# Kernel tuning notes

Hardware: AMD Instinct MI355X
Metric: run time of the kernel (lower is better)

Reference implementation:

```python
import jax, jax.numpy as jnp
import numpy as np

L = 3000          # nodes per modality
M = 3             # modalities
N = L * M         # total nodes
E = 200000        # edges
D = 512           # hidden_dim
S = D // 4        # shared_dim = 128
EPS = 1e-12       # F.normalize eps


def _lrelu(x):
    return jax.nn.leaky_relu(x, negative_slope=0.01)


def _l2norm(x):
    n = jnp.linalg.norm(x, axis=-1, keepdims=True)
    return x / jnp.maximum(n, EPS)


def setup_inputs() -> dict:
    key = jax.random.key(0)
    ks = jax.random.split(key, 16)
    w = lambda k, shape: (jax.random.normal(k, shape, dtype=jnp.float32) * 0.02)
    inp = {
        "feat0": jax.random.normal(ks[0], (L, D), dtype=jnp.float32),
        "feat1": jax.random.normal(ks[1], (L, D), dtype=jnp.float32),
        "feat2": jax.random.normal(ks[2], (L, D), dtype=jnp.float32),
        "edge_index": jax.random.randint(ks[3], (2, E), 0, N, dtype=jnp.int64),
        # EdgeWeightGen params (torch Linear convention: weight is (out, in))
        "proj_w": w(ks[4], (S, D)),
        "mlp_w1": w(ks[5], (S, 2 * S)),
        "mlp_b1": jnp.zeros((S,), dtype=jnp.float32),
        "mlp_w2": w(ks[6], (1, S)),
        "mlp_b2": jnp.zeros((1,), dtype=jnp.float32),
        # CrossModalGraphLayer params, 2 layers
        "W1_0": w(ks[7], (D, D)),
        "W2_0": w(ks[8], (D, 2 * D)),
        "W1_1": w(ks[9], (D, D)),
        "W2_1": w(ks[10], (D, 2 * D)),
    }
    return inp


def reference(feat0, feat1, feat2, edge_index, proj_w, mlp_w1, mlp_b1,
              mlp_w2, mlp_b2, W1_0, W2_0, W1_1, W2_1):
    feature = jnp.concatenate([feat0, feat1, feat2], axis=0)  # (N, D)
    src, tgt = edge_index[0], edge_index[1]

    # EdgeWeightGen
    shared_src = _l2norm(feature[src] @ proj_w.T)   # (E, S)
    shared_tgt = _l2norm(feature[tgt] @ proj_w.T)   # (E, S)
    emb_cat = jnp.concatenate([shared_src, shared_tgt], axis=-1)  # (E, 2S)
    h = _lrelu(emb_cat @ mlp_w1.T + mlp_b1)
    edge_weight = jax.nn.sigmoid((h @ mlp_w2.T + mlp_b2)[:, 0])   # (E,)

    # build_adj_matrix: dense scatter-add (sparse_coo coalesce sums dups)
    adj = jnp.zeros((N, N), dtype=feature.dtype).at[src, tgt].add(edge_weight)
    row_sum = adj.sum(axis=1)
    d_inv_sqrt = jnp.where(row_sum > 0, row_sum ** -0.5, 0.0)
    # D^{-1/2} A D^{-1/2} as elementwise row/col scaling (same math as diag matmuls)
    gcn = d_inv_sqrt[:, None] * adj * d_inv_sqrt[None, :]

    # graph layers
    x = feature
    for W1, W2 in ((W1_0, W2_0), (W1_1, W2_1)):
        proj = x @ W1.T                 # (N, D)
        nb = gcn @ proj                 # (N, D)
        cat = jnp.concatenate([x + nb, x * nb], axis=-1)  # (N, 2D)
        x = _lrelu(cat @ W2.T)
    return x  # concatenated updated features; chunk(x, 3) recovers per-modal tuple
```

## Files before the change

kernel.cpp:

```cpp
#include <hip/hip_runtime.h>
#include <hip/hip_bf16.h>
#include <math.h>

#define NL 3000
#define NN 9000
#define NE 200000
#define DD 512
#define SS 128
#define MPAD 9088
#define MT   (MPAD/16)

typedef __attribute__((ext_vector_type(8))) short    bf16x8;
typedef __attribute__((ext_vector_type(8))) ushort   u16x8;
typedef __attribute__((ext_vector_type(4))) float    f32x4;

static __device__ __forceinline__ ushort f2bf(float f){
  unsigned u = __float_as_uint(f);
  return (ushort)((u + 0x7FFFu + ((u>>16)&1u)) >> 16);
}
static __device__ __forceinline__ float bf2f(ushort u){
  return __uint_as_float(((unsigned)u)<<16);
}

__global__ __launch_bounds__(256) void k_packall(const float* __restrict__ f0, const float* __restrict__ f1,
                        const float* __restrict__ f2, const float* __restrict__ pw,
                        const float* __restrict__ w1,
                        const float* __restrict__ W10, const float* __restrict__ W20,
                        const float* __restrict__ W11, const float* __restrict__ W21,
                        const int* __restrict__ src,
                        short* __restrict__ Ap1, short* __restrict__ BpF,
                        short* __restrict__ Bp10, short* __restrict__ Bp20,
                        short* __restrict__ Bp11, short* __restrict__ Bp21,
                        short* __restrict__ Bpab,
                        float* __restrict__ row_sum, int* __restrict__ cnt){
  int b = blockIdx.x;
  int lane = threadIdx.x & 63;
  if (b < 2272){
    int t = b*4 + (threadIdx.x>>6);
    int tm = t >> 4, tk = t & 15;
    int m = tm*16 + (lane&15);
    int k = tk*32 + (lane>>4)*8;
    float4 v0 = make_float4(0,0,0,0), v1 = v0;
    if (m < NN){
      const float* srow = (m < NL) ? f0 + (size_t)m*DD
                         : (m < 2*NL) ? f1 + (size_t)(m-NL)*DD
                         : f2 + (size_t)(m-2*NL)*DD;
      v0 = *(const float4*)(srow + k);
      v1 = *(const float4*)(srow + k + 4);
    }
    u16x8 r;
    r[0]=f2bf(v0.x); r[1]=f2bf(v0.y); r[2]=f2bf(v0.z); r[3]=f2bf(v0.w);
    r[4]=f2bf(v1.x); r[5]=f2bf(v1.y); r[6]=f2bf(v1.z); r[7]=f2bf(v1.w);
    *(u16x8*)(Ap1 + (size_t)t*512 + lane*8) = r;
  } else if (b < 3072){
    int t = (b-2272)*4 + (threadIdx.x>>6);
    const float* X; short* P; int K, ntk, lt;
    if (t < 128)      { X=pw;  P=BpF;  K=512;  ntk=16; lt=t; }
    else if (t < 640) { X=W10; P=Bp10; K=512;  ntk=16; lt=t-128; }
    else if (t < 1664){ X=W20; P=Bp20; K=1024; ntk=32; lt=t-640; }
    else if (t < 2176){ X=W11; P=Bp11; K=512;  ntk=16; lt=t-1664; }
    else              { X=W21; P=Bp21; K=1024; ntk=32; lt=t-2176; }
    int tm = lt/ntk, tk = lt - tm*ntk;
    int m = tm*16 + (lane&15);
    int k = tk*32 + (lane>>4)*8;
    float4 v0 = *(const float4*)(X + (size_t)m*K + k);
    float4 v1 = *(const float4*)(X + (size_t)m*K + k + 4);
    u16x8 r;
    r[0]=f2bf(v0.x); r[1]=f2bf(v0.y); r[2]=f2bf(v0.z); r[3]=f2bf(v0.w);
    r[4]=f2bf(v1.x); r[5]=f2bf(v1.y); r[6]=f2bf(v1.z); r[7]=f2bf(v1.w);
    *(u16x8*)(P + (size_t)lt*512 + lane*8) = r;
  } else if (b < 3088){
    int t = (b-3072)*4 + (threadIdx.x>>6);
    int tn = t >> 2, tk = t & 3;
    int n = tn*16 + (lane&15);
    int k = tk*32 + (lane>>4)*8;
    const float* sp = (n<128) ? (w1 + (size_t)n*256 + k) : (w1 + (size_t)(n-128)*256 + 128 + k);
    float4 v0 = *(const float4*)sp;
    float4 v1 = *(const float4*)(sp+4);
    u16x8 r;
    r[0]=f2bf(v0.x); r[1]=f2bf(v0.y); r[2]=f2bf(v0.z); r[3]=f2bf(v0.w);
    r[4]=f2bf(v1.x); r[5]=f2bf(v1.y); r[6]=f2bf(v1.z); r[7]=f2bf(v1.w);
    *(u16x8*)(Bpab + (size_t)t*512 + lane*8) = r;
  } else {
    int idx = (b-3088)*256 + threadIdx.x;
    for (int i=idx; i<NN; i+=8192) row_sum[i]=0.f;
    for (int e=idx; e<NE; e+=8192) atomicAdd(&cnt[src[e]],1);
  }
}

__global__ __launch_bounds__(256) void k_pack(const float* __restrict__ X, short* __restrict__ P,
                                              int M, int K, int nTilesK){
  int t = blockIdx.x*4 + (threadIdx.x>>6);
  int lane = threadIdx.x & 63;
  int tm = t / nTilesK, tk = t - tm*nTilesK;
  int m = tm*16 + (lane&15);
  int k = tk*32 + (lane>>4)*8;
  float4 v0 = make_float4(0,0,0,0), v1 = v0;
  if (m < M){
    v0 = *(const float4*)(X + (size_t)m*K + k);
    v1 = *(const float4*)(X + (size_t)m*K + k + 4);
  }
  u16x8 r;
  r[0]=f2bf(v0.x); r[1]=f2bf(v0.y); r[2]=f2bf(v0.z); r[3]=f2bf(v0.w);
  r[4]=f2bf(v1.x); r[5]=f2bf(v1.y); r[6]=f2bf(v1.z); r[7]=f2bf(v1.w);
  *(u16x8*)(P + (size_t)t*512 + lane*8) = r;
}

template<int ACT, int OBF>
__global__ __launch_bounds__(256) void k_gmm(const short* __restrict__ Ap, const short* __restrict__ Bp,
                                             void* __restrict__ Cv, int M, int N, int K){
  int l = blockIdx.x;
  int rr = l & 7, tt = l >> 3;
  int q = tt % 9, x = tt / 9;
  int y = q*8 + rr;
  if (y >= 71) return;
  int lane = threadIdx.x & 63, wave = threadIdx.x >> 6;
  int ktiles = K >> 5;
  int bm = y*128 + wave*32;
  int bn = x*64;
  const bf16x8* a0 = (const bf16x8*)(Ap + ((size_t)((bm>>4)  ) * ktiles)*512 + lane*8);
  const bf16x8* a1 = (const bf16x8*)(Ap + ((size_t)((bm>>4)+1) * ktiles)*512 + lane*8);
  const bf16x8* b0 = (const bf16x8*)(Bp + ((size_t)((bn>>4)  ) * ktiles)*512 + lane*8);
  const bf16x8* b1 = (const bf16x8*)(Bp + ((size_t)((bn>>4)+1) * ktiles)*512 + lane*8);
  const bf16x8* b2 = (const bf16x8*)(Bp + ((size_t)((bn>>4)+2) * ktiles)*512 + lane*8);
  const bf16x8* b3 = (const bf16x8*)(Bp + ((size_t)((bn>>4)+3) * ktiles)*512 + lane*8);
  f32x4 acc[2][4];
  #pragma unroll
  for (int i=0;i<2;++i)
    #pragma unroll
    for (int j=0;j<4;++j) acc[i][j] = (f32x4){0.f,0.f,0.f,0.f};

  for (int kt=0; kt<ktiles; ++kt){
    int off = kt*64;
    bf16x8 A0 = a0[off], A1 = a1[off];
    bf16x8 B0 = b0[off], B1 = b1[off], B2 = b2[off], B3 = b3[off];
    acc[0][0] = __builtin_amdgcn_mfma_f32_16x16x32_bf16(A0, B0, acc[0][0], 0,0,0);
    acc[0][1] = __builtin_amdgcn_mfma_f32_16x16x32_bf16(A0, B1, acc[0][1], 0,0,0);
    acc[0][2] = __builtin_amdgcn_mfma_f32_16x16x32_bf16(A0, B2, acc[0][2], 0,0,0);
    acc[0][3] = __builtin_amdgcn_mfma_f32_16x16x32_bf16(A0, B3, acc[0][3], 0,0,0);
    acc[1][0] = __builtin_amdgcn_mfma_f32_16x16x32_bf16(A1, B0, acc[1][0], 0,0,0);
    acc[1][1] = __builtin_amdgcn_mfma_f32_16x16x32_bf16(A1, B1, acc[1][1], 0,0,0);
    acc[1][2] = __builtin_amdgcn_mfma_f32_16x16x32_bf16(A1, B2, acc[1][2], 0,0,0);
    acc[1][3] = __builtin_amdgcn_mfma_f32_16x16x32_bf16(A1, B3, acc[1][3], 0,0,0);
  }
  int colo = lane & 15;
  int rowo = (lane >> 4) * 4;
  #pragma unroll
  for (int mi=0; mi<2; ++mi){
    #pragma unroll
    for (int r=0; r<4; ++r){
      int row = bm + mi*16 + rowo + r;
      if (row < M){
        #pragma unroll
        for (int ni=0; ni<4; ++ni){
          float v = acc[mi][ni][r];
          if (ACT) v = v>0.f ? v : 0.01f*v;
          int cidx = bn + ni*16 + colo;
          if (OBF) ((ushort*)Cv)[(size_t)row*N + cidx] = f2bf(v);
          else     ((float*) Cv)[(size_t)row*N + cidx] = v;
        }
      }
    }
  }
}

__global__ __launch_bounds__(256) void k_l2n(const float* __restrict__ X, short* __restrict__ ShP){
  int lane = threadIdx.x & 63, wave = threadIdx.x >> 6;
  int m = blockIdx.x*4 + wave;
  float2 v = ((const float2*)(X + (size_t)m*SS))[lane];
  float ss = v.x*v.x + v.y*v.y;
  #pragma unroll
  for (int o=32;o>0;o>>=1) ss += __shfl_xor(ss, o);
  float inv = 1.f / fmaxf(sqrtf(ss), 1e-12f);
  int k = 2*lane;
  int tIdx = (m>>4)*4 + (k>>5);
  int pos  = ((m&15) + ((k>>3)&3)*16)*8 + (k&7);
  ushort2 r; r.x = f2bf(v.x*inv); r.y = f2bf(v.y*inv);
  *(ushort2*)(ShP + (size_t)tIdx*512 + pos) = r;
}

__global__ __launch_bounds__(256) void k_edge(const int* __restrict__ src, const int* __restrict__ tgt,
                      const ushort* __restrict__ AB,
                      const float* __restrict__ b1, const float* __restrict__ w2,
                      const float* __restrict__ b2p,
                      const int* __restrict__ row_ptr, int* __restrict__ fill,
                      int* __restrict__ col, float* __restrict__ ewC,
                      float* __restrict__ row_sum){
  int lane = threadIdx.x & 63;
  int p = lane & 15, g = lane >> 4;
  int wid = blockIdx.x*(blockDim.x>>6) + (threadIdx.x>>6);
  int nw  = gridDim.x*(blockDim.x>>6);
  float4 b1a = ((const float4*)b1)[p*2], b1b = ((const float4*)b1)[p*2+1];
  float4 w2a = ((const float4*)w2)[p*2], w2b = ((const float4*)w2)[p*2+1];
  float bb[8] = {b1a.x,b1a.y,b1a.z,b1a.w,b1b.x,b1b.y,b1b.z,b1b.w};
  float ww[8] = {w2a.x,w2a.y,w2a.z,w2a.w,w2b.x,w2b.y,w2b.z,w2b.w};
  float b2 = b2p[0];
  for (int e = wid*4+g; e < NE; e += nw*4){
    int s = src[e], tg_ = tgt[e];
    u16x8 av = *(const u16x8*)(AB + (size_t)s*256 + p*8);
    u16x8 bv = *(const u16x8*)(AB + (size_t)tg_*256 + 128 + p*8);
    float acc = 0.f;
    #pragma unroll
    for (int i=0;i<8;++i){
      float h = bf2f(av[i]) + bf2f(bv[i]) + bb[i];
      h = h>0.f ? h : 0.01f*h;
      acc += h*ww[i];
    }
    acc += __shfl_xor(acc,1); acc += __shfl_xor(acc,2);
    acc += __shfl_xor(acc,4); acc += __shfl_xor(acc,8);
    if (p==0){
      float wgt = 1.f/(1.f+expf(-(acc+b2)));
      int pos = atomicAdd(&fill[s],1);
      int idx = row_ptr[s]+pos;
      col[idx]=tg_;
      ewC[idx]=wgt;
      atomicAdd(&row_sum[s], wgt);
    }
  }
}

__global__ __launch_bounds__(1024) void k_scan(const int* __restrict__ cnt,
                      int* __restrict__ row_ptr, int* __restrict__ fill){
  __shared__ int wsum[16];
  int t = threadIdx.x;
  int lane = t & 63, wid = t >> 6;
  const int CH = 9;
  int base = t*CH;
  int v[CH]; int s = 0;
  #pragma unroll
  for (int i=0;i<CH;++i){
    int idx = base+i;
    v[i] = (idx<NN) ? cnt[idx] : 0;
    s += v[i];
  }
  int ps = s;
  #pragma unroll
  for (int o=1;o<64;o<<=1){
    int x = __shfl_up(ps, o);
    if (lane >= o) ps += x;
  }
  if (lane==63) wsum[wid] = ps;
  __syncthreads();
  if (wid==0){
    int wv = (lane<16)? wsum[lane] : 0;
    #pragma unroll
    for (int o=1;o<16;o<<=1){
      int x = __shfl_up(wv, o);
      if (lane>=o) wv += x;
    }
    if (lane<16) wsum[lane]=wv;
  }
  __syncthreads();
  int prefix = (wid>0 ? wsum[wid-1] : 0) + (ps - s);
  #pragma unroll
  for (int i=0;i<CH;++i){
    int idx = base+i;
    if (idx<NN){
      row_ptr[idx] = prefix;
      fill[idx] = 0;
      prefix += v[i];
    }
  }
  if (t==1023) row_ptr[NN] = wsum[15];
}

template<int LAYER>
__global__ __launch_bounds__(128) void k_spmm_cat(const int* __restrict__ row_ptr, const int* __restrict__ col,
                     const float* __restrict__ ew, const float* __restrict__ row_sum,
                     const ushort* __restrict__ proj,
                     const float* __restrict__ xf0, const float* __restrict__ xf1,
                     const float* __restrict__ xf2,
                     short* __restrict__ P){
  int m = blockIdx.x, t = threadIdx.x;
  int beg = row_ptr[m], end = row_ptr[m+1];
  float rsm = row_sum[m];
  float dim = rsm>0.f ? rsqrtf(rsm) : 0.f;
  float4 a0 = make_float4(0,0,0,0), a1 = a0, a2 = a0, a3 = a0;
  int j = beg;
  for (; j+4<=end; j+=4){
    int c0=col[j], c1=col[j+1], c2=col[j+2], c3=col[j+3];
    float r0=row_sum[c0], r1=row_sum[c1], r2=row_sum[c2], r3=row_sum[c3];
    float w0=ew[j]  *(r0>0.f?rsqrtf(r0):0.f);
    float w1=ew[j+1]*(r1>0.f?rsqrtf(r1):0.f);
    float w2_=ew[j+2]*(r2>0.f?rsqrtf(r2):0.f);
    float w3=ew[j+3]*(r3>0.f?rsqrtf(r3):0.f);
    ushort4 p0 = ((const ushort4*)(proj + (size_t)c0*DD))[t];
    ushort4 p1 = ((const ushort4*)(proj + (size_t)c1*DD))[t];
    ushort4 p2 = ((const ushort4*)(proj + (size_t)c2*DD))[t];
    ushort4 p3 = ((const ushort4*)(proj + (size_t)c3*DD))[t];
    a0.x += w0*bf2f(p0.x); a0.y += w0*bf2f(p0.y); a0.z += w0*bf2f(p0.z); a0.w += w0*bf2f(p0.w);
    a1.x += w1*bf2f(p1.x); a1.y += w1*bf2f(p1.y); a1.z += w1*bf2f(p1.z); a1.w += w1*bf2f(p1.w);
    a2.x += w2_*bf2f(p2.x); a2.y += w2_*bf2f(p2.y); a2.z += w2_*bf2f(p2.z); a2.w += w2_*bf2f(p2.w);
    a3.x += w3*bf2f(p3.x); a3.y += w3*bf2f(p3.y); a3.z += w3*bf2f(p3.z); a3.w += w3*bf2f(p3.w);
  }
  for (; j<end; ++j){
    int c0=col[j];
    float r0=row_sum[c0];
    float w0=ew[j]*(r0>0.f?rsqrtf(r0):0.f);
    ushort4 p0 = ((const ushort4*)(proj + (size_t)c0*DD))[t];
    a0.x += w0*bf2f(p0.x); a0.y += w0*bf2f(p0.y); a0.z += w0*bf2f(p0.z); a0.w += w0*bf2f(p0.w);
  }
  a0.x = dim*(a0.x + a1.x + a2.x + a3.x);
  a0.y = dim*(a0.y + a1.y + a2.y + a3.y);
  a0.z = dim*(a0.z + a1.z + a2.z + a3.z);
  a0.w = dim*(a0.w + a1.w + a2.w + a3.w);
  const float* xrow;
  if (LAYER==0){
    xrow = (m < NL) ? xf0 + (size_t)m*DD
         : (m < 2*NL) ? xf1 + (size_t)(m-NL)*DD
         : xf2 + (size_t)(m-2*NL)*DD;
  } else {
    xrow = xf0 + (size_t)m*DD;
  }
  float4 xv = ((const float4*)xrow)[t];
  float ax = xv.x + a0.x, ay = xv.y + a0.y, az = xv.z + a0.z, aw = xv.w + a0.w;
  float mx = xv.x * a0.x, my = xv.y * a0.y, mz = xv.z * a0.z, mw = xv.w * a0.w;
  ushort4 ra, rm;
  ra.x=f2bf(ax); ra.y=f2bf(ay); ra.z=f2bf(az); ra.w=f2bf(aw);
  rm.x=f2bf(mx); rm.y=f2bf(my); rm.z=f2bf(mz); rm.w=f2bf(mw);
  size_t tileA = (size_t)((m>>4)*32 + (t>>3));
  int    off   = ((m&15) + ((t>>1)&3)*16)*8 + (t&1)*4;
  *(ushort4*)(P + tileA*512 + off)        = ra;
  *(ushort4*)(P + (tileA+16)*512 + off)   = rm;
}

extern "C" void kernel_launch(void* const* d_in, const int* in_sizes, int n_in,
                              void* d_out, int out_size, void* d_ws, size_t ws_size,
                              hipStream_t stream){
  const float* f0 = (const float*)d_in[0];
  const float* f1 = (const float*)d_in[1];
  const float* f2 = (const float*)d_in[2];
  const int*   ei = (const int*)d_in[3];
  const float* pw = (const float*)d_in[4];
  const float* w1 = (const float*)d_in[5];
  const float* b1 = (const float*)d_in[6];
  const float* w2 = (const float*)d_in[7];
  const float* b2 = (const float*)d_in[8];
  const float* W1_0 = (const float*)d_in[9];
  const float* W2_0 = (const float*)d_in[10];
  const float* W1_1 = (const float*)d_in[11];
  const float* W2_1 = (const float*)d_in[12];
  float* out = (float*)d_out;

  const int* src = ei;
  const int* tgt = ei + NE;

  char* base = (char*)d_ws;
  size_t o = 0;
  auto alloc = [&](size_t bytes)->char*{ char* p = base + o; o += (bytes + 1023) & ~size_t(1023); return p; };
  float* x1      = (float*)alloc((size_t)NN*DD*4);
  ushort* projbf = (ushort*)alloc((size_t)NN*DD*2);
  float* projS   = (float*)alloc((size_t)NN*SS*4);
  ushort* ABn    = (ushort*)alloc((size_t)NN*256*2);
  short* Apack1  = (short*)alloc((size_t)MT*16*1024);
  short* Apack2  = (short*)alloc((size_t)MT*32*1024);
  short* ShP     = (short*)alloc((size_t)MT*4*1024);
  short* BpF     = (short*)alloc((size_t)8*16*1024);
  short* Bpab    = (short*)alloc((size_t)16*4*1024);
  short* Bp10    = (short*)alloc((size_t)32*16*1024);
  short* Bp20    = (short*)alloc((size_t)32*32*1024);
  short* Bp11    = (short*)alloc((size_t)32*16*1024);
  short* Bp21    = (short*)alloc((size_t)32*32*1024);
  float* ew      = (float*)alloc(NE*4);
  float* row_sum = (float*)alloc(NN*4);
  int*   cnt     = (int*)alloc(NN*4);
  int*   fill    = (int*)alloc(NN*4);
  int*   row_ptr = (int*)alloc((NN+1)*4);
  int*   col     = (int*)alloc(NE*4);

  hipMemsetAsync(cnt, 0, NN*4, stream);

  k_packall<<<3120, 256, 0, stream>>>(f0,f1,f2,pw,w1,W1_0,W2_0,W1_1,W2_1,src,
                                      Apack1,BpF,Bp10,Bp20,Bp11,Bp21,Bpab,row_sum,cnt);
  k_scan<<<1, 1024, 0, stream>>>(cnt,row_ptr,fill);

  k_gmm<0,0><<<2*72, 256, 0, stream>>>(Apack1, BpF, projS, NN, 128, 512);
  k_l2n<<<NN/4, 256, 0, stream>>>(projS, ShP);
  k_gmm<0,1><<<4*72, 256, 0, stream>>>(ShP, Bpab, ABn, NN, 256, 128);

  k_edge<<<2048, 256, 0, stream>>>(src,tgt,ABn,b1,w2,b2,row_ptr,fill,col,ew,row_sum);

  k_gmm<0,1><<<8*72, 256, 0, stream>>>(Apack1, Bp10, projbf, NN, DD, DD);
  k_spmm_cat<0><<<NN, 128, 0, stream>>>(row_ptr, col, ew, row_sum, projbf, f0, f1, f2, Apack2);
  k_gmm<1,0><<<8*72, 256, 0, stream>>>(Apack2, Bp20, x1, NN, DD, 2*DD);
  k_pack<<<MT*16/4, 256, 0, stream>>>(x1, Apack1, NN, DD, 16);
  k_gmm<0,1><<<8*72, 256, 0, stream>>>(Apack1, Bp11, projbf, NN, DD, DD);
  k_spmm_cat<1><<<NN, 128, 0, stream>>>(row_ptr, col, ew, row_sum, projbf, x1, nullptr, nullptr, Apack2);
  k_gmm<1,0><<<8*72, 256, 0, stream>>>(Apack2, Bp21, out, NN, DD, 2*DD);
}
```

Baseline: 319.3 us.

## Fuse edge-projection GEMM, L2 norm and MLP GEMM; emit packed bf16 layer output

```diff
diff --git a/kernel.cpp b/kernel.cpp
--- a/kernel.cpp
+++ b/kernel.cpp
@@ -88,22 +88,85 @@
   }
 }
 
-__global__ __launch_bounds__(256) void k_pack(const float* __restrict__ X, short* __restrict__ P,
-                                              int M, int K, int nTilesK){
-  int t = blockIdx.x*4 + (threadIdx.x>>6);
-  int lane = threadIdx.x & 63;
-  int tm = t / nTilesK, tk = t - tm*nTilesK;
-  int m = tm*16 + (lane&15);
-  int k = tk*32 + (lane>>4)*8;
-  float4 v0 = make_float4(0,0,0,0), v1 = v0;
-  if (m < M){
-    v0 = *(const float4*)(X + (size_t)m*K + k);
-    v1 = *(const float4*)(X + (size_t)m*K + k + 4);
-  }
-  u16x8 r;
-  r[0]=f2bf(v0.x); r[1]=f2bf(v0.y); r[2]=f2bf(v0.z); r[3]=f2bf(v0.w);
-  r[4]=f2bf(v1.x); r[5]=f2bf(v1.y); r[6]=f2bf(v1.z); r[7]=f2bf(v1.w);
-  *(u16x8*)(P + (size_t)t*512 + lane*8) = r;
+__global__ __launch_bounds__(256) void k_front(const short* __restrict__ Ap, const short* __restrict__ BpF,
+                                               const short* __restrict__ Bpab, ushort* __restrict__ ABn){
+  __shared__ ushort sh[4][32][136];
+  int lane = threadIdx.x & 63, wave = threadIdx.x >> 6;
+  int bm = blockIdx.x*128 + wave*32;
+  const bf16x8* a0 = (const bf16x8*)(Ap + ((size_t)((bm>>4)  )*16)*512 + lane*8);
+  const bf16x8* a1 = (const bf16x8*)(Ap + ((size_t)((bm>>4)+1)*16)*512 + lane*8);
+  const bf16x8* bp[8];
+  #pragma unroll
+  for (int i=0;i<8;++i) bp[i] = (const bf16x8*)(BpF + ((size_t)i*16)*512 + lane*8);
+  f32x4 acc[2][8];
+  #pragma unroll
+  for (int i=0;i<2;++i)
+    #pragma unroll
+    for (int j=0;j<8;++j) acc[i][j] = (f32x4){0.f,0.f,0.f,0.f};
+  for (int kt=0; kt<16; ++kt){
+    int off = kt*64;
+    bf16x8 A0 = a0[off], A1 = a1[off];
+    #pragma unroll
+    for (int i=0;i<8;++i){
+      bf16x8 Bf = bp[i][off];
+      acc[0][i] = __builtin_amdgcn_mfma_f32_16x16x32_bf16(A0, Bf, acc[0][i], 0,0,0);
+      acc[1][i] = __builtin_amdgcn_mfma_f32_16x16x32_bf16(A1, Bf, acc[1][i], 0,0,0);
+    }
+  }
+  int rowo = (lane>>4)*4, colo = lane & 15;
+  float inv[2][4];
+  #pragma unroll
+  for (int mi=0; mi<2; ++mi){
+    #pragma unroll
+    for (int r=0; r<4; ++r){
+      float s = 0.f;
+      #pragma unroll
+      for (int ni=0; ni<8; ++ni){ float v = acc[mi][ni][r]; s += v*v; }
+      s += __shfl_xor(s,1); s += __shfl_xor(s,2); s += __shfl_xor(s,4); s += __shfl_xor(s,8);
+      inv[mi][r] = 1.f / fmaxf(sqrtf(s), 1e-12f);
+    }
+  }
+  #pragma unroll
+  for (int mi=0; mi<2; ++mi)
+    #pragma unroll
+    for (int r=0; r<4; ++r)
+      #pragma unroll
+      for (int ni=0; ni<8; ++ni)
+        sh[wave][mi*16 + rowo + r][colo + 16*ni] = f2bf(acc[mi][ni][r]*inv[mi][r]);
+  __syncthreads();
+  bf16x8 af[2][4];
+  #pragma unroll
+  for (int mi=0; mi<2; ++mi)
+    #pragma unroll
+    for (int kt=0; kt<4; ++kt)
+      af[mi][kt] = *(const bf16x8*)&sh[wave][mi*16 + (lane&15)][kt*32 + (lane>>4)*8];
+  for (int p=0; p<2; ++p){
+    #pragma unroll
+    for (int i=0;i<2;++i)
+      #pragma unroll
+      for (int j=0;j<8;++j) acc[i][j] = (f32x4){0.f,0.f,0.f,0.f};
+    #pragma unroll
+    for (int kt=0; kt<4; ++kt){
+      #pragma unroll
+      for (int ci=0; ci<8; ++ci){
+        bf16x8 Bf = *(const bf16x8*)(Bpab + ((size_t)((p*8+ci)*4 + kt))*512 + lane*8);
+        acc[0][ci] = __builtin_amdgcn_mfma_f32_16x16x32_bf16(af[0][kt], Bf, acc[0][ci], 0,0,0);
+        acc[1][ci] = __builtin_amdgcn_mfma_f32_16x16x32_bf16(af[1][kt], Bf, acc[1][ci], 0,0,0);
+      }
+    }
+    #pragma unroll
+    for (int mi=0; mi<2; ++mi){
+      #pragma unroll
+      for (int r=0; r<4; ++r){
+        int row = bm + mi*16 + rowo + r;
+        if (row < NN){
+          #pragma unroll
+          for (int ni=0; ni<8; ++ni)
+            ABn[(size_t)row*256 + p*128 + ni*16 + colo] = f2bf(acc[mi][ni][r]);
+        }
+      }
+    }
+  }
 }
 
 template<int ACT, int OBF>
@@ -156,27 +219,17 @@
           float v = acc[mi][ni][r];
           if (ACT) v = v>0.f ? v : 0.01f*v;
           int cidx = bn + ni*16 + colo;
-          if (OBF) ((ushort*)Cv)[(size_t)row*N + cidx] = f2bf(v);
-          else     ((float*) Cv)[(size_t)row*N + cidx] = v;
+          if (OBF==1)      ((ushort*)Cv)[(size_t)row*N + cidx] = f2bf(v);
+          else if (OBF==2){
+            size_t tl = (size_t)(row>>4)*16 + (cidx>>5);
+            int pos = ((row&15) + ((cidx>>3)&3)*16)*8 + (cidx&7);
+            ((ushort*)Cv)[tl*512 + pos] = f2bf(v);
+          }
+          else             ((float*) Cv)[(size_t)row*N + cidx] = v;
         }
       }
     }
   }
-}
-
-__global__ __launch_bounds__(256) void k_l2n(const float* __restrict__ X, short* __restrict__ ShP){
-  int lane = threadIdx.x & 63, wave = threadIdx.x >> 6;
-  int m = blockIdx.x*4 + wave;
-  float2 v = ((const float2*)(X + (size_t)m*SS))[lane];
-  float ss = v.x*v.x + v.y*v.y;
-  #pragma unroll
-  for (int o=32;o>0;o>>=1) ss += __shfl_xor(ss, o);
-  float inv = 1.f / fmaxf(sqrtf(ss), 1e-12f);
-  int k = 2*lane;
-  int tIdx = (m>>4)*4 + (k>>5);
-  int pos  = ((m&15) + ((k>>3)&3)*16)*8 + (k&7);
-  ushort2 r; r.x = f2bf(v.x*inv); r.y = f2bf(v.y*inv);
-  *(ushort2*)(ShP + (size_t)tIdx*512 + pos) = r;
 }
 
 __global__ __launch_bounds__(256) void k_edge(const int* __restrict__ src, const int* __restrict__ tgt,
@@ -269,7 +322,7 @@
                      const float* __restrict__ ew, const float* __restrict__ row_sum,
                      const ushort* __restrict__ proj,
                      const float* __restrict__ xf0, const float* __restrict__ xf1,
-                     const float* __restrict__ xf2,
+                     const float* __restrict__ xf2, const short* __restrict__ xp,
                      short* __restrict__ P){
   int m = blockIdx.x, t = threadIdx.x;
   int beg = row_ptr[m], end = row_ptr[m+1];
@@ -304,15 +357,17 @@
   a0.y = dim*(a0.y + a1.y + a2.y + a3.y);
   a0.z = dim*(a0.z + a1.z + a2.z + a3.z);
   a0.w = dim*(a0.w + a1.w + a2.w + a3.w);
-  const float* xrow;
+  float4 xv;
   if (LAYER==0){
-    xrow = (m < NL) ? xf0 + (size_t)m*DD
+    const float* xrow = (m < NL) ? xf0 + (size_t)m*DD
          : (m < 2*NL) ? xf1 + (size_t)(m-NL)*DD
          : xf2 + (size_t)(m-2*NL)*DD;
+    xv = ((const float4*)xrow)[t];
   } else {
-    xrow = xf0 + (size_t)m*DD;
-  }
-  float4 xv = ((const float4*)xrow)[t];
+    ushort4 xq = *(const ushort4*)(xp + ((size_t)((m>>4)*16 + (t>>3)))*512
+                                      + ((m&15) + ((t>>1)&3)*16)*8 + (t&1)*4);
+    xv = make_float4(bf2f(xq.x), bf2f(xq.y), bf2f(xq.z), bf2f(xq.w));
+  }
   float ax = xv.x + a0.x, ay = xv.y + a0.y, az = xv.z + a0.z, aw = xv.w + a0.w;
   float mx = xv.x * a0.x, my = xv.y * a0.y, mz = xv.z * a0.z, mw = xv.w * a0.w;
   ushort4 ra, rm;
@@ -348,13 +403,10 @@
   char* base = (char*)d_ws;
   size_t o = 0;
   auto alloc = [&](size_t bytes)->char*{ char* p = base + o; o += (bytes + 1023) & ~size_t(1023); return p; };
-  float* x1      = (float*)alloc((size_t)NN*DD*4);
   ushort* projbf = (ushort*)alloc((size_t)NN*DD*2);
-  float* projS   = (float*)alloc((size_t)NN*SS*4);
   ushort* ABn    = (ushort*)alloc((size_t)NN*256*2);
   short* Apack1  = (short*)alloc((size_t)MT*16*1024);
   short* Apack2  = (short*)alloc((size_t)MT*32*1024);
-  short* ShP     = (short*)alloc((size_t)MT*4*1024);
   short* BpF     = (short*)alloc((size_t)8*16*1024);
   short* Bpab    = (short*)alloc((size_t)16*4*1024);
   short* Bp10    = (short*)alloc((size_t)32*16*1024);
@@ -374,17 +426,14 @@
                                       Apack1,BpF,Bp10,Bp20,Bp11,Bp21,Bpab,row_sum,cnt);
   k_scan<<<1, 1024, 0, stream>>>(cnt,row_ptr,fill);
 
-  k_gmm<0,0><<<2*72, 256, 0, stream>>>(Apack1, BpF, projS, NN, 128, 512);
-  k_l2n<<<NN/4, 256, 0, stream>>>(projS, ShP);
-  k_gmm<0,1><<<4*72, 256, 0, stream>>>(ShP, Bpab, ABn, NN, 256, 128);
+  k_front<<<71, 256, 0, stream>>>(Apack1, BpF, Bpab, ABn);
 
   k_edge<<<2048, 256, 0, stream>>>(src,tgt,ABn,b1,w2,b2,row_ptr,fill,col,ew,row_sum);
 
   k_gmm<0,1><<<8*72, 256, 0, stream>>>(Apack1, Bp10, projbf, NN, DD, DD);
-  k_spmm_cat<0><<<NN, 128, 0, stream>>>(row_ptr, col, ew, row_sum, projbf, f0, f1, f2, Apack2);
-  k_gmm<1,0><<<8*72, 256, 0, stream>>>(Apack2, Bp20, x1, NN, DD, 2*DD);
-  k_pack<<<MT*16/4, 256, 0, stream>>>(x1, Apack1, NN, DD, 16);
+  k_spmm_cat<0><<<NN, 128, 0, stream>>>(row_ptr, col, ew, row_sum, projbf, f0, f1, f2, nullptr, Apack2);
+  k_gmm<1,2><<<8*72, 256, 0, stream>>>(Apack2, Bp20, Apack1, NN, DD, 2*DD);
   k_gmm<0,1><<<8*72, 256, 0, stream>>>(Apack1, Bp11, projbf, NN, DD, DD);
-  k_spmm_cat<1><<<NN, 128, 0, stream>>>(row_ptr, col, ew, row_sum, projbf, x1, nullptr, nullptr, Apack2);
+  k_spmm_cat<1><<<NN, 128, 0, stream>>>(row_ptr, col, ew, row_sum, projbf, nullptr, nullptr, nullptr, Apack1, Apack2);
   k_gmm<1,0><<<8*72, 256, 0, stream>>>(Apack2, Bp21, out, NN, DD, 2*DD);
 }
```

New measurement: 321.6 us. About the same (+0.7%).
